# Performance work log

Hardware: AMD Instinct MI355X
Metric: run time of the kernel (lower is better)

The kernel has to match this reference:

```python
import jax, jax.numpy as jnp
import numpy as np

# DCNv2 config (matches init_kwargs)
STRIDE, PAD, DIL = 1, 1, 1
KH, KW = 3, 3
K = KH * KW


def setup_inputs() -> dict:
    key = jax.random.key(0)
    k1, k2, k3, k4 = jax.random.split(key, 4)
    B, C, H, W = 2, 256, 96, 96
    O = 256
    inp = jax.random.normal(k1, (B, C, H, W), jnp.float32)
    # offset channels interleaved (dy, dx) per kernel tap -> 2*K channels
    offset = jax.random.normal(k2, (B, 2 * K, H, W), jnp.float32)
    # modulation mask in [0,1) (sigmoid is applied outside this module in DCN heads)
    mask = jax.random.uniform(k3, (B, K, H, W), jnp.float32)
    n = C * KH * KW
    stdv = 1.0 / float(np.sqrt(n))
    weight = jax.random.uniform(k4, (O, C, KH, KW), jnp.float32, -stdv, stdv)
    bias = jnp.zeros((O,), jnp.float32)
    return {"input": inp, "offset": offset, "mask": mask, "weight": weight, "bias": bias}


def reference(input, offset, mask, weight, bias):
    B, C, H, W = input.shape
    O = weight.shape[0]
    Ho = (H + 2 * PAD - DIL * (KH - 1) - 1) // STRIDE + 1
    Wo = (W + 2 * PAD - DIL * (KW - 1) - 1) // STRIDE + 1

    # learned per-pixel offsets: channel layout [dy_k0, dx_k0, dy_k1, dx_k1, ...]
    dy = offset[:, 0::2]  # [B,K,Ho,Wo]
    dx = offset[:, 1::2]  # [B,K,Ho,Wo]

    ky = (jnp.arange(K) // KW * DIL).astype(jnp.float32)  # kernel tap row offsets
    kx = (jnp.arange(K) % KW * DIL).astype(jnp.float32)   # kernel tap col offsets
    base_y = (jnp.arange(Ho) * STRIDE - PAD).astype(jnp.float32)
    base_x = (jnp.arange(Wo) * STRIDE - PAD).astype(jnp.float32)

    # sampling positions, [B,K,Ho,Wo]
    y = base_y[None, None, :, None] + ky[None, :, None, None] + dy
    x = base_x[None, None, None, :] + kx[None, :, None, None] + dx

    y0 = jnp.floor(y)
    x0 = jnp.floor(x)
    wy = y - y0  # bilinear fractional weights
    wx = x - x0

    inp_flat = input.reshape(B, C, H * W)

    def gather(yi, xi):
        # zero-padded bilinear corner gather: out-of-bounds -> 0
        ii = yi.astype(jnp.int32)
        jj = xi.astype(jnp.int32)
        valid = ((ii >= 0) & (ii < H) & (jj >= 0) & (jj < W)).astype(input.dtype)
        idx = jnp.clip(ii, 0, H - 1) * W + jnp.clip(jj, 0, W - 1)  # [B,K,Ho,Wo]
        v = jnp.take_along_axis(inp_flat, idx.reshape(B, 1, -1), axis=2)  # [B,C,K*Ho*Wo]
        return v * valid.reshape(B, 1, -1)

    v00 = gather(y0, x0)
    v01 = gather(y0, x0 + 1)
    v10 = gather(y0 + 1, x0)
    v11 = gather(y0 + 1, x0 + 1)

    wyf = wy.reshape(B, 1, -1)
    wxf = wx.reshape(B, 1, -1)
    sampled = (v00 * (1 - wyf) * (1 - wxf) + v01 * (1 - wyf) * wxf
               + v10 * wyf * (1 - wxf) + v11 * wyf * wxf)  # [B,C,K*Ho*Wo]

    mod = sampled * mask.reshape(B, 1, -1)           # modulation per tap/pixel
    mod = mod.reshape(B, C, K, Ho * Wo)
    out = jnp.einsum('bcks,ock->bos', mod, weight.reshape(O, C, K)) + bias[None, :, None]
    return out.reshape(B, O, Ho, Wo)
```

## Files before the change

### kernel.cpp

```cpp
#include <hip/hip_runtime.h>
#include <hip/hip_bf16.h>


#define Hh 96
#define Ww 96
#define Cc 256
#define Oo 256
#define Bb 2
#define Kk 9
#define Ss (Hh * Ww)
#define CKTOT (Cc * Kk)

typedef __bf16 bf16x8 __attribute__((ext_vector_type(8)));
typedef __bf16 bf16x4v __attribute__((ext_vector_type(4)));
typedef __bf16 bf16x2v __attribute__((ext_vector_type(2)));
typedef float f32x4 __attribute__((ext_vector_type(4)));
typedef float f32x2 __attribute__((ext_vector_type(2)));

__device__ __forceinline__ f32x2 up2(unsigned u) {
  f32x2 r;
  r.x = __uint_as_float(u << 16);
  r.y = __uint_as_float(u & 0xffff0000u);
  return r;
}

__device__ __forceinline__ void barrier_lgkm() {
  asm volatile("" ::: "memory");
  __builtin_amdgcn_s_waitcnt(0xC07F);
  __builtin_amdgcn_s_barrier();
  asm volatile("" ::: "memory");
}

__global__ __launch_bounds__(256) void prep(const float* __restrict__ inp,
                                            const float* __restrict__ wsrc,
                                            __bf16* __restrict__ it,
                                            __bf16* __restrict__ wt) {
  __shared__ float tile[64][65];
  const int bx = blockIdx.x;
  const int tid = threadIdx.x;

  if (bx < 1152) {
    const int hw0 = (bx % 144) * 64;
    const int c0 = ((bx / 144) & 3) * 64;
    const int b = bx / 576;
    const int hw_l = tid & 63, cr = tid >> 6;
    const float* src = inp + ((size_t)(b * Cc + c0) * Ss) + hw0;
#pragma unroll
    for (int r = 0; r < 16; ++r) {
      int c_l = r * 4 + cr;
      tile[c_l][hw_l] = src[(size_t)c_l * Ss + hw_l];
    }
    __syncthreads();
    const int cp = (tid & 31) * 2, hr = tid >> 5;
    __bf16* dst = it + ((size_t)(b * Ss + hw0) * Cc) + c0;
#pragma unroll
    for (int r = 0; r < 8; ++r) {
      int hw_s = r * 8 + hr;
      bf16x2v p;
      p.x = (__bf16)tile[cp][hw_s];
      p.y = (__bf16)tile[cp + 1][hw_s];
      *(bf16x2v*)(dst + (size_t)hw_s * Cc + cp) = p;
    }
  } else {
    int i = (bx - 1152) * 256 + tid;
    int j = i & 7;
    int l = (i >> 3) & 63;
    int osub = (i >> 9) & 15;
    int cc = (i >> 13) & 7;
    int kk = i >> 16;
    int o = osub * 16 + (l & 15);
    int ch = cc * 32 + ((l >> 4) << 3) + j;
    wt[i] = (__bf16)wsrc[(o * Cc + ch) * Kk + kk];
  }
}

__global__ __launch_bounds__(512, 4) void dcn_main(
    const __bf16* __restrict__ it,
    const __bf16* __restrict__ wt,
    const float* __restrict__ offset,
    const float* __restrict__ mask,
    const float* __restrict__ bias,
    float* __restrict__ out)
{
  __shared__ __bf16 colT[2][64][48];
  __shared__ int4 pa9[9][64];
  __shared__ float4 pw9[9][64];

  const int tid = threadIdx.x;
  const int tile = (blockIdx.x & 7) * 18 + (blockIdx.x >> 3);
  const int s0 = tile * 64;
  const int bo = blockIdx.y;
  const int b = blockIdx.z;
  const int lane = tid & 63;
  const int wv = tid >> 6;
  const int quad = lane >> 4;
  const int l15 = lane & 15;
  const int sg = tid >> 3;
  const int cg = tid & 7;

  const __bf16* itb = it + (size_t)b * Ss * Cc;

  for (int idx = tid; idx < 9 * 64; idx += 512) {
    int kk = idx >> 6;
    int sl = idx & 63;
    int s = s0 + sl;
    int ho = s / Ww;
    int wo = s - ho * Ww;
    float dy = offset[((size_t)(b * 18 + 2 * kk)) * Ss + s];
    float dx = offset[((size_t)(b * 18 + 2 * kk + 1)) * Ss + s];
    float m = mask[((size_t)(b * 9 + kk)) * Ss + s];
    float y = (float)(ho - 1 + kk / 3) + dy;
    float x = (float)(wo - 1 + kk % 3) + dx;
    float fy = floorf(y), fx = floorf(x);
    int y0 = (int)fy, x0 = (int)fx;
    float wy = y - fy, wx = x - fx;
    int y1 = y0 + 1, x1 = x0 + 1;
    float vy0 = (y0 >= 0 && y0 < Hh) ? 1.f : 0.f;
    float vy1 = (y1 >= 0 && y1 < Hh) ? 1.f : 0.f;
    float vx0 = (x0 >= 0 && x0 < Ww) ? 1.f : 0.f;
    float vx1 = (x1 >= 0 && x1 < Ww) ? 1.f : 0.f;
    int y0c = min(max(y0, 0), Hh - 1), y1c = min(max(y1, 0), Hh - 1);
    int x0c = min(max(x0, 0), Ww - 1), x1c = min(max(x1, 0), Ww - 1);
    pa9[kk][sl] = make_int4((y0c * Ww + x0c) * Cc, (y0c * Ww + x1c) * Cc,
                            (y1c * Ww + x0c) * Cc, (y1c * Ww + x1c) * Cc);
    pw9[kk][sl] = make_float4(m * (1.f - wy) * (1.f - wx) * vy0 * vx0,
                              m * (1.f - wy) * wx * vy0 * vx1,
                              m * wy * (1.f - wx) * vy1 * vx0,
                              m * wy * wx * vy1 * vx1);
  }
  __syncthreads();

  f32x4 acc[4];
#pragma unroll
  for (int j = 0; j < 4; ++j) acc[j] = (f32x4){0.f, 0.f, 0.f, 0.f};

  uint2 D[2][4];
  float4 PW[2];
  bf16x8 W[2];

  auto pf_data = [&](int i, int ph) {
    int kk = i >> 3, ccb = (i & 7) << 5;
    int4 a = pa9[kk][sg];
    PW[ph] = pw9[kk][sg];
    const __bf16* bp = itb + (ccb + (cg << 2));
    D[ph][0] = *(const uint2*)(bp + a.x);
    D[ph][1] = *(const uint2*)(bp + a.y);
    D[ph][2] = *(const uint2*)(bp + a.z);
    D[ph][3] = *(const uint2*)(bp + a.w);
  };
  auto pf_w = [&](int i, int ph) {
    int kk = i >> 3, cc = i & 7;
    int osub = bo * 8 + wv;
    W[ph] = *(const bf16x8*)(wt + (((size_t)((kk * 8 + cc) * 16 + osub)) << 9) + lane * 8);
  };

  auto step = [&](int i, int cur, int nxt) {
    {
      float4 wq = PW[cur];
      f32x2 r01 = up2(D[cur][0].x) * wq.x + up2(D[cur][1].x) * wq.y +
                  up2(D[cur][2].x) * wq.z + up2(D[cur][3].x) * wq.w;
      f32x2 r23 = up2(D[cur][0].y) * wq.x + up2(D[cur][1].y) * wq.y +
                  up2(D[cur][2].y) * wq.z + up2(D[cur][3].y) * wq.w;
      bf16x4v rv;
      rv.x = (__bf16)r01.x;
      rv.y = (__bf16)r01.y;
      rv.z = (__bf16)r23.x;
      rv.w = (__bf16)r23.y;
      *(bf16x4v*)&colT[cur][sg][cg << 2] = rv;
    }
    if (i < 71) {
      pf_data(i + 1, nxt);
      pf_w(i + 1, nxt);
    }
    barrier_lgkm();
    bf16x8 bfr[4];
#pragma unroll
    for (int st = 0; st < 4; ++st)
      bfr[st] = *(const bf16x8*)(&colT[cur][st * 16 + l15][quad * 8]);
#pragma unroll
    for (int st = 0; st < 4; ++st)
      acc[st] = __builtin_amdgcn_mfma_f32_16x16x32_bf16(W[cur], bfr[st], acc[st], 0, 0, 0);
  };

  pf_data(0, 0);
  pf_w(0, 0);
  for (int ii = 0; ii < 72; ii += 2) {
    step(ii, 0, 1);
    step(ii + 1, 1, 0);
  }

  int obase = bo * 128 + wv * 16 + quad * 4;
#pragma unroll
  for (int r = 0; r < 4; ++r) {
    int o = obase + r;
    float bi = bias[o];
    float* op = out + ((size_t)(b * Oo + o)) * Ss + s0 + l15;
#pragma unroll
    for (int st = 0; st < 4; ++st) {
      op[st * 16] = acc[st][r] + bi;
    }
  }
}

extern "C" void kernel_launch(void* const* d_in, const int* in_sizes, int n_in,
                              void* d_out, int out_size, void* d_ws, size_t ws_size,
                              hipStream_t stream) {
  (void)in_sizes; (void)n_in; (void)out_size; (void)ws_size;
  const float* inp = (const float*)d_in[0];
  const float* offset = (const float*)d_in[1];
  const float* mask = (const float*)d_in[2];
  const float* weight = (const float*)d_in[3];
  const float* bias = (const float*)d_in[4];
  float* out = (float*)d_out;

  __bf16* it = (__bf16*)d_ws;
  __bf16* wt = (__bf16*)((char*)d_ws + (size_t)Bb * Ss * Cc * 2);

  prep<<<3456, 256, 0, stream>>>(inp, weight, it, wt);
  dcn_main<<<dim3(144, 2, Bb), 512, 0, stream>>>(it, wt, offset, mask, bias, out);
}
```

Baseline: 154.7 us.

## Restructure DCN main kernel to 32-pixel tiles with 32x32 MFMA and full-channel slabs

Each block now covers 32 output pixels and all 256 output channels, instead of splitting output channels across two blocks. Per kernel tap, the full 256-channel bilinear-sampled slab is built in XOR-swizzled shared memory. The accumulation then uses 32x32x16 bf16 MFMAs with two accumulators per wave, and the weight layout is repacked to match. This removes the duplicated gather and interpolation work across output-channel blocks and cuts barriers from 72 to 9. In exchange, gather loads are no longer prefetched across barriers, so loads and MFMAs overlap less and occupancy may drop.

```diff
diff --git a/kernel.cpp b/kernel.cpp
--- a/kernel.cpp
+++ b/kernel.cpp
@@ -12,9 +12,8 @@
 #define CKTOT (Cc * Kk)
 
 typedef __bf16 bf16x8 __attribute__((ext_vector_type(8)));
-typedef __bf16 bf16x4v __attribute__((ext_vector_type(4)));
 typedef __bf16 bf16x2v __attribute__((ext_vector_type(2)));
-typedef float f32x4 __attribute__((ext_vector_type(4)));
+typedef float f32x16 __attribute__((ext_vector_type(16)));
 typedef float f32x2 __attribute__((ext_vector_type(2)));
 
 __device__ __forceinline__ f32x2 up2(unsigned u) {
@@ -65,16 +64,16 @@
     int i = (bx - 1152) * 256 + tid;
     int j = i & 7;
     int l = (i >> 3) & 63;
-    int osub = (i >> 9) & 15;
-    int cc = (i >> 13) & 7;
+    int osub = (i >> 9) & 7;
+    int cc = (i >> 12) & 15;
     int kk = i >> 16;
-    int o = osub * 16 + (l & 15);
-    int ch = cc * 32 + ((l >> 4) << 3) + j;
+    int o = osub * 32 + (l & 31);
+    int ch = cc * 16 + ((l >> 5) << 3) + j;
     wt[i] = (__bf16)wsrc[(o * Cc + ch) * Kk + kk];
   }
 }
 
-__global__ __launch_bounds__(512, 4) void dcn_main(
+__global__ __launch_bounds__(256, 3) void dcn_main(
     const __bf16* __restrict__ it,
     const __bf16* __restrict__ wt,
     const float* __restrict__ offset,
@@ -82,27 +81,26 @@
     const float* __restrict__ bias,
     float* __restrict__ out)
 {
-  __shared__ __bf16 colT[2][64][48];
-  __shared__ int4 pa9[9][64];
-  __shared__ float4 pw9[9][64];
+  __shared__ __bf16 colT[2][32 * 256];
+  __shared__ int4 pa9[9][32];
+  __shared__ float4 pw9[9][32];
 
   const int tid = threadIdx.x;
-  const int tile = (blockIdx.x & 7) * 18 + (blockIdx.x >> 3);
-  const int s0 = tile * 64;
-  const int bo = blockIdx.y;
-  const int b = blockIdx.z;
+  const int tile = (blockIdx.x & 7) * 36 + (blockIdx.x >> 3);
+  const int s0 = tile * 32;
+  const int b = blockIdx.y;
   const int lane = tid & 63;
   const int wv = tid >> 6;
-  const int quad = lane >> 4;
-  const int l15 = lane & 15;
-  const int sg = tid >> 3;
-  const int cg = tid & 7;
+  const int sB = lane & 31;
+  const int hi = lane >> 5;
+  const int fs = tid >> 3;
+  const int fg = tid & 7;
 
   const __bf16* itb = it + (size_t)b * Ss * Cc;
 
-  for (int idx = tid; idx < 9 * 64; idx += 512) {
-    int kk = idx >> 6;
-    int sl = idx & 63;
+  for (int idx = tid; idx < 9 * 32; idx += 256) {
+    int kk = idx >> 5;
+    int sl = idx & 31;
     int s = s0 + sl;
     int ho = s / Ww;
     int wo = s - ho * Ww;
@@ -130,74 +128,79 @@
   }
   __syncthreads();
 
-  f32x4 acc[4];
-#pragma unroll
-  for (int j = 0; j < 4; ++j) acc[j] = (f32x4){0.f, 0.f, 0.f, 0.f};
-
-  uint2 D[2][4];
-  float4 PW[2];
-  bf16x8 W[2];
-
-  auto pf_data = [&](int i, int ph) {
-    int kk = i >> 3, ccb = (i & 7) << 5;
-    int4 a = pa9[kk][sg];
-    PW[ph] = pw9[kk][sg];
-    const __bf16* bp = itb + (ccb + (cg << 2));
-    D[ph][0] = *(const uint2*)(bp + a.x);
-    D[ph][1] = *(const uint2*)(bp + a.y);
-    D[ph][2] = *(const uint2*)(bp + a.z);
-    D[ph][3] = *(const uint2*)(bp + a.w);
+  f32x16 acc0, acc1;
+#pragma unroll
+  for (int j = 0; j < 16; ++j) { acc0[j] = 0.f; acc1[j] = 0.f; }
+
+  auto ldW = [&](int kk, int cc, int which) {
+    size_t idx = (size_t)((kk * 16 + cc) * 8 + wv * 2 + which);
+    return *(const bf16x8*)(wt + (idx << 9) + (lane << 3));
   };
-  auto pf_w = [&](int i, int ph) {
-    int kk = i >> 3, cc = i & 7;
-    int osub = bo * 8 + wv;
-    W[ph] = *(const bf16x8*)(wt + (((size_t)((kk * 8 + cc) * 16 + osub)) << 9) + lane * 8);
+  auto ldB = [&](int buf, int cc) {
+    int g = ((2 * cc + hi) ^ (sB & 7)) << 3;
+    return *(const bf16x8*)(&colT[buf][sB * 256 + g]);
   };
 
-  auto step = [&](int i, int cur, int nxt) {
+  for (int kk = 0; kk < Kk; ++kk) {
+    const int buf = kk & 1;
     {
-      float4 wq = PW[cur];
-      f32x2 r01 = up2(D[cur][0].x) * wq.x + up2(D[cur][1].x) * wq.y +
-                  up2(D[cur][2].x) * wq.z + up2(D[cur][3].x) * wq.w;
-      f32x2 r23 = up2(D[cur][0].y) * wq.x + up2(D[cur][1].y) * wq.y +
-                  up2(D[cur][2].y) * wq.z + up2(D[cur][3].y) * wq.w;
-      bf16x4v rv;
-      rv.x = (__bf16)r01.x;
-      rv.y = (__bf16)r01.y;
-      rv.z = (__bf16)r23.x;
-      rv.w = (__bf16)r23.y;
-      *(bf16x4v*)&colT[cur][sg][cg << 2] = rv;
-    }
-    if (i < 71) {
-      pf_data(i + 1, nxt);
-      pf_w(i + 1, nxt);
-    }
+      int4 a = pa9[kk][fs];
+      float4 wq = pw9[kk][fs];
+      __bf16* drow = &colT[buf][fs * 256];
+#pragma unroll
+      for (int it2 = 0; it2 < 4; ++it2) {
+        int g = fg + it2 * 8;
+        const __bf16* p = itb + g * 8;
+        uint4 c00 = *(const uint4*)(p + a.x);
+        uint4 c01 = *(const uint4*)(p + a.y);
+        uint4 c10 = *(const uint4*)(p + a.z);
+        uint4 c11 = *(const uint4*)(p + a.w);
+        unsigned u0[4] = {c00.x, c00.y, c00.z, c00.w};
+        unsigned u1[4] = {c01.x, c01.y, c01.z, c01.w};
+        unsigned u2[4] = {c10.x, c10.y, c10.z, c10.w};
+        unsigned u3[4] = {c11.x, c11.y, c11.z, c11.w};
+        bf16x8 rv;
+#pragma unroll
+        for (int w = 0; w < 4; ++w) {
+          f32x2 r = up2(u0[w]) * wq.x + up2(u1[w]) * wq.y +
+                    up2(u2[w]) * wq.z + up2(u3[w]) * wq.w;
+          rv[2 * w] = (__bf16)r.x;
+          rv[2 * w + 1] = (__bf16)r.y;
+        }
+        *(bf16x8*)(drow + ((g ^ (fs & 7)) << 3)) = rv;
+      }
+    }
+    bf16x8 Wacur = ldW(kk, 0, 0);
+    bf16x8 Wbcur = ldW(kk, 0, 1);
     barrier_lgkm();
-    bf16x8 bfr[4];
-#pragma unroll
-    for (int st = 0; st < 4; ++st)
-      bfr[st] = *(const bf16x8*)(&colT[cur][st * 16 + l15][quad * 8]);
-#pragma unroll
-    for (int st = 0; st < 4; ++st)
-      acc[st] = __builtin_amdgcn_mfma_f32_16x16x32_bf16(W[cur], bfr[st], acc[st], 0, 0, 0);
-  };
-
-  pf_data(0, 0);
-  pf_w(0, 0);
-  for (int ii = 0; ii < 72; ii += 2) {
-    step(ii, 0, 1);
-    step(ii + 1, 1, 0);
-  }
-
-  int obase = bo * 128 + wv * 16 + quad * 4;
-#pragma unroll
-  for (int r = 0; r < 4; ++r) {
-    int o = obase + r;
-    float bi = bias[o];
-    float* op = out + ((size_t)(b * Oo + o)) * Ss + s0 + l15;
-#pragma unroll
-    for (int st = 0; st < 4; ++st) {
-      op[st * 16] = acc[st][r] + bi;
+
+    bf16x8 Bcur = ldB(buf, 0);
+#pragma unroll
+    for (int cc = 0; cc < 16; ++cc) {
+      bf16x8 Bn, Wan, Wbn;
+      if (cc < 15) {
+        Bn = ldB(buf, cc + 1);
+        Wan = ldW(kk, cc + 1, 0);
+        Wbn = ldW(kk, cc + 1, 1);
+      }
+      acc0 = __builtin_amdgcn_mfma_f32_32x32x16_bf16(Wacur, Bcur, acc0, 0, 0, 0);
+      acc1 = __builtin_amdgcn_mfma_f32_32x32x16_bf16(Wbcur, Bcur, acc1, 0, 0, 0);
+      if (cc < 15) {
+        Bcur = Bn;
+        Wacur = Wan;
+        Wbcur = Wbn;
+      }
+    }
+  }
+
+  float* ob = out + (size_t)b * Oo * Ss + s0 + sB;
+#pragma unroll
+  for (int os = 0; os < 2; ++os) {
+#pragma unroll
+    for (int r = 0; r < 16; ++r) {
+      int o = wv * 64 + os * 32 + (r & 3) + 8 * (r >> 2) + 4 * hi;
+      float v = (os ? acc1[r] : acc0[r]) + bias[o];
+      ob[(size_t)o * Ss] = v;
     }
   }
 }
@@ -217,5 +220,5 @@
   __bf16* wt = (__bf16*)((char*)d_ws + (size_t)Bb * Ss * Cc * 2);
 
   prep<<<3456, 256, 0, stream>>>(inp, weight, it, wt);
-  dcn_main<<<dim3(144, 2, Bb), 512, 0, stream>>>(it, wt, offset, mask, bias, out);
-}
+  dcn_main<<<dim3(288, Bb), 256, 0, stream>>>(it, wt, offset, mask, bias, out);
+}
```

Result: faster. 128.1 us (-17.2%).
